# Kernel tuning notes

Measured on AMD Instinct MI355X. Metric: run time of the kernel, lower is better.

Reference implementation:

```python
import jax, jax.numpy as jnp
import numpy as np

D_MODEL = 256
N_HEADS = 4
SPARSITY_RATIO = 0.5
B, N, E = 4, 2048, 65536


def setup_inputs() -> dict:
    key = jax.random.key(0)
    ks = jax.random.split(key, 16)
    d, h = D_MODEL, D_MODEL // 2
    s = 1.0 / np.sqrt(d)
    inp = {
        "x": jax.random.normal(ks[0], (B, N, d), dtype=jnp.float32),
        "edge_index": jax.random.randint(ks[1], (2, E), 0, N, dtype=jnp.int64),
        "Wq": jax.random.uniform(ks[2], (d, d), minval=-s, maxval=s),
        "bq": jnp.zeros((d,), jnp.float32),
        "Wk": jax.random.uniform(ks[3], (d, d), minval=-s, maxval=s),
        "bk": jnp.zeros((d,), jnp.float32),
        "Wv": jax.random.uniform(ks[4], (d, d), minval=-s, maxval=s),
        "bv": jnp.zeros((d,), jnp.float32),
        "Wo": jax.random.uniform(ks[5], (d, d), minval=-s, maxval=s),
        "bo": jnp.zeros((d,), jnp.float32),
        "Wg1": jax.random.uniform(ks[6], (d, h), minval=-s, maxval=s),  # gnn conv1 (in,out)
        "bg1": jnp.zeros((h,), jnp.float32),
        "Wg2": jax.random.uniform(ks[7], (h, 1), minval=-s, maxval=s),  # gnn conv2
        "bg2": jnp.zeros((1,), jnp.float32),
    }
    return inp


def reference(x, edge_index, Wq, bq, Wk, bk, Wv, bv, Wo, bo, Wg1, bg1, Wg2, bg2):
    b, n, d = x.shape
    hd = d // N_HEADS
    row, col = edge_index[0], edge_index[1]

    # Lightweight GNN topo scores, vmapped over batch (replaces python loop)
    def gnn(xb):
        aggr = jax.ops.segment_sum(xb[col], row, num_segments=n)  # [N, d]
        hdn = jax.nn.relu(aggr @ Wg1 + bg1)
        return (hdn @ Wg2 + bg2)[:, 0]  # [N]

    topo_scores = jax.vmap(gnn)(x)  # [B, N]

    Q = (x @ Wq + bq).reshape(b, n, N_HEADS, hd)
    K = (x @ Wk + bk).reshape(b, n, N_HEADS, hd)
    V = (x @ Wv + bv).reshape(b, n, N_HEADS, hd)

    content_scores = jnp.einsum('bnhd,bmhd->bhnm', Q, K) / np.sqrt(hd)
    content_attn = jax.nn.softmax(content_scores, axis=-1)  # [B,H,N,N]

    # Edge mask (identical across batch, assignment semantics => set)
    edge_mask = jnp.zeros((n, n), jnp.float32).at[row, col].set(1.0)

    # top-k columns per batch (same columns for every query row i)
    k = max(1, int(n * (1 - SPARSITY_RATIO)))
    _, topk_idx = jax.lax.top_k(topo_scores, k)  # [B, k]
    col_mask = jnp.zeros((b, n), jnp.float32).at[jnp.arange(b)[:, None], topk_idx].set(1.0)

    sparse_mask = jnp.maximum(edge_mask[None, :, :], col_mask[:, None, :])  # [B,N,N]
    mask4 = jnp.broadcast_to(sparse_mask[:, None, :, :], (b, N_HEADS, n, n))

    sparse_attn = content_attn * mask4
    sparse_attn = sparse_attn / (jnp.sum(sparse_attn, axis=-1, keepdims=True) + 1e-8)

    out = jnp.einsum('bhnm,bmhd->bnhd', sparse_attn, V).reshape(b, n, d)
    out = out @ Wo + bo
    return out, mask4
```

## Files before the change

### kernel.cpp

```cpp
#include <hip/hip_runtime.h>
#include <hip/hip_bf16.h>
#include <stdint.h>

#define NTOK 2048
#define NB 4
#define DM 256
#define HD 64
#define NE 65536
#define SCAP 128
#define NKSL 4
#define LIVE_ROWS 6272

typedef __bf16 bf16x8 __attribute__((ext_vector_type(8)));
typedef float f32x4 __attribute__((ext_vector_type(4)));

#define MFMA16 __builtin_amdgcn_mfma_f32_16x16x32_bf16

__device__ __forceinline__ unsigned short f2bf(float f) {
    union { float f; uint32_t u; } v; v.f = f;
    return (unsigned short)((v.u + 0x7fffu + ((v.u >> 16) & 1u)) >> 16);
}

__global__ __launch_bounds__(256) void k_prep(const float* __restrict__ x,
                       unsigned short* __restrict__ xb,
                       const float* __restrict__ W0, const float* __restrict__ W1,
                       const float* __restrict__ W2, const float* __restrict__ W3,
                       unsigned short* __restrict__ WT, float4* __restrict__ wsz,
                       const float* __restrict__ Wg1, float* __restrict__ y) {
    __shared__ float xs[16][256];
    int bid = blockIdx.x, t = threadIdx.x;
    if (bid < 132) {
        wsz[bid * 256 + t] = float4{0.f, 0.f, 0.f, 0.f};
    } else if (bid < 1156) {
        int b2 = bid - 132;
        int sel = b2 >> 8;
        const float* W = sel == 0 ? W0 : sel == 1 ? W1 : sel == 2 ? W2 : W3;
        int e = (b2 & 255) * 256 + t;
        int n = e >> 8, k = e & 255;
        WT[sel * 65536 + e] = f2bf(W[k * 256 + n]);
    } else {
        int m0 = (bid - 1156) * 16;
        #pragma unroll
        for (int j = 0; j < 16; ++j) {
            float v = x[(size_t)(m0 + j) * DM + t];
            xs[j][t] = v;
            xb[(size_t)(m0 + j) * DM + t] = f2bf(v);
        }
        __syncthreads();
        int c = t & 127, g = t >> 7;
        float acc[8] = {0.f, 0.f, 0.f, 0.f, 0.f, 0.f, 0.f, 0.f};
        const float* xr = &xs[g * 8][0];
        #pragma unroll 4
        for (int r = 0; r < DM; ++r) {
            float w = Wg1[r * 128 + c];
            #pragma unroll
            for (int j = 0; j < 8; ++j) acc[j] += xr[j * 256 + r] * w;
        }
        #pragma unroll
        for (int j = 0; j < 8; ++j) y[(size_t)(m0 + g * 8 + j) * 128 + c] = acc[j];
    }
}

__global__ void k_edges(const int* __restrict__ ei, uint32_t* __restrict__ cursor,
                        uint32_t* __restrict__ scol, uint32_t* __restrict__ ebits) {
    int e = blockIdx.x * 256 + threadIdx.x;
    int r = ei[e];
    int c = ei[NE + e];
    uint32_t slot = atomicAdd(&cursor[r], 1u);
    if (slot < SCAP) scol[r * SCAP + slot] = (uint32_t)c;
    atomicOr(&ebits[r * 64 + (c >> 5)], 1u << (c & 31));
}

__global__ __launch_bounds__(256) void k_gnn_qkv(
    const float* __restrict__ y, const uint32_t* __restrict__ cursor,
    const uint32_t* __restrict__ scol,
    const float* __restrict__ bg1, const float* __restrict__ Wg2,
    const float* __restrict__ bg2, float* __restrict__ topo,
    const unsigned short* __restrict__ xbf, const unsigned short* __restrict__ WT,
    const float* __restrict__ bq, const float* __restrict__ bk, const float* __restrict__ bv,
    unsigned short* __restrict__ qo, unsigned short* __restrict__ kt,
    unsigned short* __restrict__ vt3) {
    int bid = blockIdx.x, t = threadIdx.x;
    if (bid < 2048) {
        int i = bid;
        int d = t & 127, bp = t >> 7;
        uint32_t cnt = cursor[i]; if (cnt > SCAP) cnt = SCAP;
        const uint32_t* sc = scol + i * SCAP;
        const float* yA = y + (size_t)(bp * NTOK) * 128 + d;
        const float* yB = y + (size_t)((bp + 2) * NTOK) * 128 + d;
        double A0 = 0, A1 = 0, A2 = 0, A3 = 0;
        double B0 = 0, B1 = 0, B2 = 0, B3 = 0;
        uint32_t e = 0;
        for (; e + 3 < cnt; e += 4) {
            int c0 = sc[e] << 7, c1 = sc[e + 1] << 7;
            int c2 = sc[e + 2] << 7, c3 = sc[e + 3] << 7;
            A0 += (double)yA[c0]; A1 += (double)yA[c1];
            A2 += (double)yA[c2]; A3 += (double)yA[c3];
            B0 += (double)yB[c0]; B1 += (double)yB[c1];
            B2 += (double)yB[c2]; B3 += (double)yB[c3];
        }
        for (; e < cnt; ++e) {
            int c0 = sc[e] << 7;
            A0 += (double)yA[c0];
            B0 += (double)yB[c0];
        }
        double hA = (A0 + A1) + (A2 + A3) + (double)bg1[d];
        double hB = (B0 + B1) + (B2 + B3) + (double)bg1[d];
        double w2 = (double)Wg2[d];
        double vA = (hA > 0 ? hA : 0.0) * w2;
        double vB = (hB > 0 ? hB : 0.0) * w2;
        #pragma unroll
        for (int s = 32; s >= 1; s >>= 1) {
            vA += __shfl_xor(vA, s);
            vB += __shfl_xor(vB, s);
        }
        __shared__ double red[4][2];
        int wid = t >> 6;
        if ((t & 63) == 0) { red[wid][0] = vA; red[wid][1] = vB; }
        __syncthreads();
        if (t == 0) {
            double bb = (double)bg2[0];
            topo[0 * NTOK + i] = (float)(red[0][0] + red[1][0] + bb);
            topo[2 * NTOK + i] = (float)(red[0][1] + red[1][1] + bb);
            topo[1 * NTOK + i] = (float)(red[2][0] + red[3][0] + bb);
            topo[3 * NTOK + i] = (float)(red[2][1] + red[3][1] + bb);
        }
    } else {
        int b2 = bid - 2048;
        int z = b2 >> 9, r2 = b2 & 511;
        const unsigned short* W = WT + z * 65536;
        const float* bias = z == 0 ? bq : z == 1 ? bk : bv;

        int lane = t & 63, w = t >> 6;
        int l15 = lane & 15, grp = lane >> 4;
        int mbase = (r2 & 127) * 64 + w * 16;
        int nbase = (r2 >> 7) * 64;
        f32x4 acc0 = {0,0,0,0}, acc1 = {0,0,0,0}, acc2 = {0,0,0,0}, acc3 = {0,0,0,0};
        const unsigned short* ap = xbf + (size_t)(mbase + l15) * DM + grp * 8;
        const unsigned short* bp2 = W + (size_t)(nbase + l15) * DM + grp * 8;
        #pragma unroll
        for (int k0 = 0; k0 < DM; k0 += 32) {
            bf16x8 af = *(const bf16x8*)(ap + k0);
            acc0 = MFMA16(af, *(const bf16x8*)(bp2 + k0), acc0, 0, 0, 0);
            acc1 = MFMA16(af, *(const bf16x8*)(bp2 + 16 * DM + k0), acc1, 0, 0, 0);
            acc2 = MFMA16(af, *(const bf16x8*)(bp2 + 32 * DM + k0), acc2, 0, 0, 0);
            acc3 = MFMA16(af, *(const bf16x8*)(bp2 + 48 * DM + k0), acc3, 0, 0, 0);
        }
        f32x4 accs[4] = {acc0, acc1, acc2, acc3};
        #pragma unroll
        for (int ct = 0; ct < 4; ++ct) {
            #pragma unroll
            for (int r = 0; r < 4; ++r) {
                int m = mbase + grp * 4 + r;
                int n = nbase + ct * 16 + l15;
                float v = accs[ct][r] + bias[n];
                if (z == 0) {
                    qo[(size_t)m * DM + n] = f2bf(v);
                } else {
                    int b = m >> 11, tok = m & 2047, h = n >> 6, d = n & 63;
                    int bh = (b << 2) + h;
                    if (z == 1) {
                        kt[(size_t)bh * 131072 + (tok >> 4) * 1024 + (tok & 15) * 64 + d] = f2bf(v);
                    } else {
                        vt3[(size_t)bh * 131072 + (tok >> 5) * 2048 + d * 32 + (tok & 31)] = f2bf(v);
                    }
                }
            }
        }
    }
}

__global__ __launch_bounds__(256) void k_topk(const float* __restrict__ topo,
                                              uint32_t* __restrict__ colbits) {
    int b = blockIdx.y, t = threadIdx.x;
    int i = blockIdx.x * 256 + t;
    __shared__ float4 sc4[NTOK / 4];
    const float4* tp = (const float4*)(topo + b * NTOK);
    for (int j = t; j < NTOK / 4; j += 256) sc4[j] = tp[j];
    __syncthreads();
    float si = ((const float*)sc4)[i];
    int rank = 0;
    #pragma unroll 2
    for (int jj = 0; jj < NTOK / 4; ++jj) {
        float4 v = sc4[jj];
        int j0 = jj * 4;
        rank += (v.x > si) || (v.x == si && (j0    ) < i);
        rank += (v.y > si) || (v.y == si && (j0 + 1) < i);
        rank += (v.z > si) || (v.z == si && (j0 + 2) < i);
        rank += (v.w > si) || (v.w == si && (j0 + 3) < i);
    }
    unsigned long long m = __ballot(rank < 1024);
    int lane = t & 63;
    if (lane == 0)       colbits[b * 64 + (i >> 5)] = (uint32_t)m;
    else if (lane == 32) colbits[b * 64 + (i >> 5)] = (uint32_t)(m >> 32);
}

__device__ __forceinline__ void mask_row(int rowidx, const uint32_t* __restrict__ eb,
                                         const uint32_t* __restrict__ cb,
                                         float* __restrict__ mout) {
    int t = threadIdx.x;
    int b = rowidx >> 13;
    int i = rowidx & 2047;
    int j0 = t << 3;
    uint32_t mw = eb[i * 64 + (j0 >> 5)] | cb[b * 64 + (j0 >> 5)];
    int sh = j0 & 31;
    float4 v0, v1;
    v0.x = ((mw >> sh) & 1u) ? 1.f : 0.f;
    v0.y = ((mw >> (sh + 1)) & 1u) ? 1.f : 0.f;
    v0.z = ((mw >> (sh + 2)) & 1u) ? 1.f : 0.f;
    v0.w = ((mw >> (sh + 3)) & 1u) ? 1.f : 0.f;
    v1.x = ((mw >> (sh + 4)) & 1u) ? 1.f : 0.f;
    v1.y = ((mw >> (sh + 5)) & 1u) ? 1.f : 0.f;
    v1.z = ((mw >> (sh + 6)) & 1u) ? 1.f : 0.f;
    v1.w = ((mw >> (sh + 7)) & 1u) ? 1.f : 0.f;
    float* p = mout + (size_t)rowidx * NTOK + j0;
    *(float4*)p = v0;
    *(float4*)(p + 4) = v1;
}

__global__ __launch_bounds__(256) void k_attn_mask(const unsigned short* __restrict__ Q,
                                                   const unsigned short* __restrict__ KT,
                                                   const unsigned short* __restrict__ VT3,
                                                   const uint32_t* __restrict__ ebits,
                                                   const uint32_t* __restrict__ colbits,
                                                   float* __restrict__ po,
                                                   float* __restrict__ pl,
                                                   float* __restrict__ mout) {
    int bid = blockIdx.x;
    if (bid >= 2048) {
        mask_row(bid - 2048 + LIVE_ROWS, ebits, colbits, mout);
        return;
    }
    int lane = threadIdx.x & 63, w = threadIdx.x >> 6;
    int l15 = lane & 15, grp = lane >> 4;
    int ks = bid >> 9;
    int bh = (bid >> 5) & 15, b = bh >> 2, h = bh & 3;
    int q = (bid & 31) * 64 + w * 16 + l15;

    const unsigned short* qp = Q + (size_t)(b * NTOK + q) * DM + h * HD + grp * 8;
    bf16x8 qf0 = *(const bf16x8*)(qp);
    bf16x8 qf1 = *(const bf16x8*)(qp + 32);
    const unsigned short* kbase = KT + (size_t)bh * 131072 + l15 * 64 + grp * 8;
    const unsigned short* vbase = VT3 + (size_t)bh * 131072 + l15 * 32 + grp * 8;
    const uint32_t* eb = ebits + q * 64;
    const uint32_t* cbp = colbits + b * 64;

    f32x4 o0 = {0,0,0,0}, o1 = {0,0,0,0}, o2 = {0,0,0,0}, o3 = {0,0,0,0};
    float psum = 0.f;

    int kb0 = ks * (NTOK / NKSL);
    for (int kb = kb0; kb < kb0 + NTOK / NKSL; kb += 32) {
        const unsigned short* kp0 = kbase + (kb >> 4) * 1024;
        f32x4 st0 = {0,0,0,0}, st1 = {0,0,0,0};
        st0 = MFMA16(*(const bf16x8*)(kp0), qf0, st0, 0, 0, 0);
        st0 = MFMA16(*(const bf16x8*)(kp0 + 32), qf1, st0, 0, 0, 0);
        st1 = MFMA16(*(const bf16x8*)(kp0 + 1024), qf0, st1, 0, 0, 0);
        st1 = MFMA16(*(const bf16x8*)(kp0 + 1024 + 32), qf1, st1, 0, 0, 0);

        uint32_t mw = eb[kb >> 5] | cbp[kb >> 5];
        float p[8];
        #pragma unroll
        for (int r = 0; r < 4; ++r) {
            int p0 = grp * 4 + r;
            p[r]     = ((mw >> p0) & 1u)        ? __expf(st0[r] * 0.125f - 8.0f) : 0.f;
            p[4 + r] = ((mw >> (16 + p0)) & 1u) ? __expf(st1[r] * 0.125f - 8.0f) : 0.f;
        }
        #pragma unroll
        for (int j = 0; j < 8; ++j) psum += p[j];

        uint32_t pk00, pk01, pk10, pk11;
        asm("v_cvt_pk_bf16_f32 %0, %1, %2" : "=v"(pk00) : "v"(p[0]), "v"(p[1]));
        asm("v_cvt_pk_bf16_f32 %0, %1, %2" : "=v"(pk01) : "v"(p[2]), "v"(p[3]));
        asm("v_cvt_pk_bf16_f32 %0, %1, %2" : "=v"(pk10) : "v"(p[4]), "v"(p[5]));
        asm("v_cvt_pk_bf16_f32 %0, %1, %2" : "=v"(pk11) : "v"(p[6]), "v"(p[7]));
        union { uint32_t u[4]; bf16x8 v; } pf;
        #pragma unroll
        for (int wi = 0; wi < 4; ++wi) {
            int src = (((grp * 2 + (wi >> 1)) & 3) << 4) | l15;
            uint32_t lo = (uint32_t)__shfl((int)((wi & 1) ? pk01 : pk00), src);
            uint32_t hi = (uint32_t)__shfl((int)((wi & 1) ? pk11 : pk10), src);
            pf.u[wi] = (lane >= 32) ? hi : lo;
        }

        const unsigned short* vk = vbase + (kb >> 5) * 2048;
        o0 = MFMA16(*(const bf16x8*)(vk),            pf.v, o0, 0, 0, 0);
        o1 = MFMA16(*(const bf16x8*)(vk + 16 * 32),  pf.v, o1, 0, 0, 0);
        o2 = MFMA16(*(const bf16x8*)(vk + 32 * 32),  pf.v, o2, 0, 0, 0);
        o3 = MFMA16(*(const bf16x8*)(vk + 48 * 32),  pf.v, o3, 0, 0, 0);
    }
    psum += __shfl_xor(psum, 16);
    psum += __shfl_xor(psum, 32);

    float* pb = po + (((size_t)(ks * 16 + bh) * NTOK + q) * HD);
    *(f32x4*)(pb + 0 * 16 + grp * 4) = o0;
    *(f32x4*)(pb + 1 * 16 + grp * 4) = o1;
    *(f32x4*)(pb + 2 * 16 + grp * 4) = o2;
    *(f32x4*)(pb + 3 * 16 + grp * 4) = o3;
    if (grp == 0) pl[(size_t)(ks * 16 + bh) * NTOK + q] = psum;
}

__global__ __launch_bounds__(256) void k_fin(const float* __restrict__ po,
                                             const float* __restrict__ pl,
                                             unsigned short* __restrict__ aoutb) {
    const size_t SL = (size_t)16 * NTOK * HD;
    const size_t SLP = (size_t)16 * NTOK;
    int tid = blockIdx.x * 256 + threadIdx.x;
    int dc = tid & 7;
    int q = (tid >> 3) & 2047;
    int bh = tid >> 14;
    size_t rb = ((size_t)bh * NTOK + q) * HD + dc * 8;
    float4 s0 = *(const float4*)(po + rb);
    float4 s1 = *(const float4*)(po + rb + 4);
    #pragma unroll
    for (int ks = 1; ks < NKSL; ++ks) {
        float4 a = *(const float4*)(po + ks * SL + rb);
        float4 c = *(const float4*)(po + ks * SL + rb + 4);
        s0.x += a.x; s0.y += a.y; s0.z += a.z; s0.w += a.w;
        s1.x += c.x; s1.y += c.y; s1.z += c.z; s1.w += c.w;
    }
    float l = 0.f;
    #pragma unroll
    for (int ks = 0; ks < NKSL; ++ks) l += pl[ks * SLP + (size_t)bh * NTOK + q];
    float inv = 1.f / l;
    int b = bh >> 2, h = bh & 3;
    union { ushort4 u4[2]; uint4 v; } out;
    out.u4[0].x = f2bf(s0.x * inv); out.u4[0].y = f2bf(s0.y * inv);
    out.u4[0].z = f2bf(s0.z * inv); out.u4[0].w = f2bf(s0.w * inv);
    out.u4[1].x = f2bf(s1.x * inv); out.u4[1].y = f2bf(s1.y * inv);
    out.u4[1].z = f2bf(s1.z * inv); out.u4[1].w = f2bf(s1.w * inv);
    *(uint4*)(aoutb + ((size_t)(b * NTOK + q) * DM) + h * HD + dc * 8) = out.v;
}

__global__ __launch_bounds__(256) void k_gemm_o(const unsigned short* __restrict__ A,
                                                const unsigned short* __restrict__ WT,
                                                const float* __restrict__ bias,
                                                float* __restrict__ out) {
    int bid = blockIdx.x;
    int lane = threadIdx.x & 63, w = threadIdx.x >> 6;
    int l15 = lane & 15, grp = lane >> 4;
    int mbase = (bid & 127) * 64 + w * 16;
    int nbase = (bid >> 7) * 64;
    f32x4 acc0 = {0,0,0,0}, acc1 = {0,0,0,0}, acc2 = {0,0,0,0}, acc3 = {0,0,0,0};
    const unsigned short* ap = A + (size_t)(mbase + l15) * DM + grp * 8;
    const unsigned short* bp = WT + (size_t)(nbase + l15) * DM + grp * 8;
    #pragma unroll
    for (int k0 = 0; k0 < DM; k0 += 32) {
        bf16x8 af = *(const bf16x8*)(ap + k0);
        acc0 = MFMA16(af, *(const bf16x8*)(bp + k0), acc0, 0, 0, 0);
        acc1 = MFMA16(af, *(const bf16x8*)(bp + 16 * DM + k0), acc1, 0, 0, 0);
        acc2 = MFMA16(af, *(const bf16x8*)(bp + 32 * DM + k0), acc2, 0, 0, 0);
        acc3 = MFMA16(af, *(const bf16x8*)(bp + 48 * DM + k0), acc3, 0, 0, 0);
    }
    f32x4 accs[4] = {acc0, acc1, acc2, acc3};
    #pragma unroll
    for (int ct = 0; ct < 4; ++ct) {
        #pragma unroll
        for (int r = 0; r < 4; ++r) {
            int m = mbase + grp * 4 + r;
            int n = nbase + ct * 16 + l15;
            out[(size_t)m * DM + n] = accs[ct][r] + bias[n];
        }
    }
}

__global__ void k_mask4b(const uint32_t* __restrict__ ebits, const uint32_t* __restrict__ colbits,
                         float* __restrict__ mout) {
    mask_row(blockIdx.x, ebits, colbits, mout);
}

extern "C" void kernel_launch(void* const* d_in, const int* in_sizes, int n_in,
                              void* d_out, int out_size, void* d_ws, size_t ws_size,
                              hipStream_t stream) {
    const float* x   = (const float*)d_in[0];
    const int*   ei  = (const int*)d_in[1];
    const float* Wq  = (const float*)d_in[2];
    const float* bq  = (const float*)d_in[3];
    const float* Wk  = (const float*)d_in[4];
    const float* bk  = (const float*)d_in[5];
    const float* Wv  = (const float*)d_in[6];
    const float* bv  = (const float*)d_in[7];
    const float* Wo  = (const float*)d_in[8];
    const float* bo  = (const float*)d_in[9];
    const float* Wg1 = (const float*)d_in[10];
    const float* bg1 = (const float*)d_in[11];
    const float* Wg2 = (const float*)d_in[12];
    const float* bg2 = (const float*)d_in[13];

    float* out0  = (float*)d_out;
    float* mask4 = out0 + (size_t)NB * NTOK * DM;

    uint8_t* big = (uint8_t*)mask4;
    unsigned short* qbf   = (unsigned short*)(big);
    unsigned short* kt    = (unsigned short*)(big + (4u  << 20));
    unsigned short* vt3   = (unsigned short*)(big + (8u  << 20));
    unsigned short* wt    = (unsigned short*)(big + (12u << 20));
    unsigned short* aoutb = (unsigned short*)(big + (12u << 20) + (512u << 10));
    float*          po    = (float*)(big + (16u << 20) + (512u << 10));
    float*          pl    = (float*)(big + (48u << 20) + (512u << 10));
    unsigned short* xbf   = (unsigned short*)(big + (49u << 20));
    uint32_t*       scol  = (uint32_t*)(big + (53u << 20));
    float*          y     = (float*)(big + (54u << 20));

    uint8_t* ws = (uint8_t*)d_ws;
    uint32_t* cursor  = (uint32_t*)(ws);
    uint32_t* ebits   = (uint32_t*)(ws + (16u << 10));
    uint32_t* colbits = (uint32_t*)(ws + (528u << 10));
    float*    topo    = (float*)(ws + (532u << 10));

    k_prep<<<1668, 256, 0, stream>>>(x, xbf, Wq, Wk, Wv, Wo, wt, (float4*)ws, Wg1, y);
    k_edges<<<256, 256, 0, stream>>>(ei, cursor, scol, ebits);
    k_gnn_qkv<<<3584, 256, 0, stream>>>(y, cursor, scol, bg1, Wg2, bg2, topo,
                                        xbf, wt, bq, bk, bv, qbf, kt, vt3);
    k_topk<<<dim3(8, 4), 256, 0, stream>>>(topo, colbits);
    k_attn_mask<<<2048 + (32768 - LIVE_ROWS), 256, 0, stream>>>(qbf, kt, vt3, ebits, colbits,
                                                                po, pl, mask4);
    k_fin<<<1024, 256, 0, stream>>>(po, pl, aoutb);
    k_gemm_o<<<512, 256, 0, stream>>>(aoutb, wt + 196608, bo, out0);
    k_mask4b<<<LIVE_ROWS, 256, 0, stream>>>(ebits, colbits, mask4);
}
```

Before: 302.5 us.

## Stage K/V tiles in swizzled shared memory and write mask once per head-quad

```diff
diff --git a/kernel.cpp b/kernel.cpp
--- a/kernel.cpp
+++ b/kernel.cpp
@@ -9,7 +9,6 @@
 #define NE 65536
 #define SCAP 128
 #define NKSL 4
-#define LIVE_ROWS 6272
 
 typedef __bf16 bf16x8 __attribute__((ext_vector_type(8)));
 typedef float f32x4 __attribute__((ext_vector_type(4)));
@@ -195,43 +194,18 @@
     else if (lane == 32) colbits[b * 64 + (i >> 5)] = (uint32_t)(m >> 32);
 }
 
-__device__ __forceinline__ void mask_row(int rowidx, const uint32_t* __restrict__ eb,
-                                         const uint32_t* __restrict__ cb,
-                                         float* __restrict__ mout) {
-    int t = threadIdx.x;
-    int b = rowidx >> 13;
-    int i = rowidx & 2047;
-    int j0 = t << 3;
-    uint32_t mw = eb[i * 64 + (j0 >> 5)] | cb[b * 64 + (j0 >> 5)];
-    int sh = j0 & 31;
-    float4 v0, v1;
-    v0.x = ((mw >> sh) & 1u) ? 1.f : 0.f;
-    v0.y = ((mw >> (sh + 1)) & 1u) ? 1.f : 0.f;
-    v0.z = ((mw >> (sh + 2)) & 1u) ? 1.f : 0.f;
-    v0.w = ((mw >> (sh + 3)) & 1u) ? 1.f : 0.f;
-    v1.x = ((mw >> (sh + 4)) & 1u) ? 1.f : 0.f;
-    v1.y = ((mw >> (sh + 5)) & 1u) ? 1.f : 0.f;
-    v1.z = ((mw >> (sh + 6)) & 1u) ? 1.f : 0.f;
-    v1.w = ((mw >> (sh + 7)) & 1u) ? 1.f : 0.f;
-    float* p = mout + (size_t)rowidx * NTOK + j0;
-    *(float4*)p = v0;
-    *(float4*)(p + 4) = v1;
-}
-
-__global__ __launch_bounds__(256) void k_attn_mask(const unsigned short* __restrict__ Q,
+__global__ __launch_bounds__(256) void k_attn_part(const unsigned short* __restrict__ Q,
                                                    const unsigned short* __restrict__ KT,
                                                    const unsigned short* __restrict__ VT3,
                                                    const uint32_t* __restrict__ ebits,
                                                    const uint32_t* __restrict__ colbits,
                                                    float* __restrict__ po,
-                                                   float* __restrict__ pl,
-                                                   float* __restrict__ mout) {
+                                                   float* __restrict__ pl) {
+    __shared__ unsigned short ksh[2][2048];
+    __shared__ unsigned short vsh[2][2048];
     int bid = blockIdx.x;
-    if (bid >= 2048) {
-        mask_row(bid - 2048 + LIVE_ROWS, ebits, colbits, mout);
-        return;
-    }
-    int lane = threadIdx.x & 63, w = threadIdx.x >> 6;
+    int t = threadIdx.x;
+    int lane = t & 63, w = t >> 6;
     int l15 = lane & 15, grp = lane >> 4;
     int ks = bid >> 9;
     int bh = (bid >> 5) & 15, b = bh >> 2, h = bh & 3;
@@ -240,22 +214,46 @@
     const unsigned short* qp = Q + (size_t)(b * NTOK + q) * DM + h * HD + grp * 8;
     bf16x8 qf0 = *(const bf16x8*)(qp);
     bf16x8 qf1 = *(const bf16x8*)(qp + 32);
-    const unsigned short* kbase = KT + (size_t)bh * 131072 + l15 * 64 + grp * 8;
-    const unsigned short* vbase = VT3 + (size_t)bh * 131072 + l15 * 32 + grp * 8;
+    const unsigned short* Kt = KT + (size_t)bh * 131072;
+    const unsigned short* Vt = VT3 + (size_t)bh * 131072;
     const uint32_t* eb = ebits + q * 64;
     const uint32_t* cbp = colbits + b * 64;
 
+    int kb0 = ks * (NTOK / NKSL);
+
+    int kso = (t * 16) ^ (((t >> 3) & 7) << 4);
+    int vso = (t * 16) ^ (((t >> 2) & 7) << 4);
+    int swz = (l15 & 7) << 4;
+
+    {
+        uint4 kv = *(const uint4*)(Kt + (size_t)(kb0 >> 4) * 1024 + t * 8);
+        *(uint4*)((char*)&ksh[0][0] + kso) = kv;
+        uint4 vv = *(const uint4*)(Vt + (size_t)(kb0 >> 5) * 2048 + t * 8);
+        *(uint4*)((char*)&vsh[0][0] + vso) = vv;
+    }
+    __syncthreads();
+
     f32x4 o0 = {0,0,0,0}, o1 = {0,0,0,0}, o2 = {0,0,0,0}, o3 = {0,0,0,0};
     float psum = 0.f;
 
-    int kb0 = ks * (NTOK / NKSL);
-    for (int kb = kb0; kb < kb0 + NTOK / NKSL; kb += 32) {
-        const unsigned short* kp0 = kbase + (kb >> 4) * 1024;
+    for (int it = 0; it < NTOK / NKSL / 32; ++it) {
+        int buf = it & 1;
+        if (it + 1 < NTOK / NKSL / 32) {
+            int kb = kb0 + (it + 1) * 32;
+            uint4 kv = *(const uint4*)(Kt + (size_t)(kb >> 4) * 1024 + t * 8);
+            *(uint4*)((char*)&ksh[buf ^ 1][0] + kso) = kv;
+            uint4 vv = *(const uint4*)(Vt + (size_t)(kb >> 5) * 2048 + t * 8);
+            *(uint4*)((char*)&vsh[buf ^ 1][0] + vso) = vv;
+        }
+        int kb = kb0 + it * 32;
+        const char* kp = (const char*)&ksh[buf][0];
+        const char* vp = (const char*)&vsh[buf][0];
+
         f32x4 st0 = {0,0,0,0}, st1 = {0,0,0,0};
-        st0 = MFMA16(*(const bf16x8*)(kp0), qf0, st0, 0, 0, 0);
-        st0 = MFMA16(*(const bf16x8*)(kp0 + 32), qf1, st0, 0, 0, 0);
-        st1 = MFMA16(*(const bf16x8*)(kp0 + 1024), qf0, st1, 0, 0, 0);
-        st1 = MFMA16(*(const bf16x8*)(kp0 + 1024 + 32), qf1, st1, 0, 0, 0);
+        st0 = MFMA16(*(const bf16x8*)(kp + ((l15 * 128 + grp * 16) ^ swz)),        qf0, st0, 0, 0, 0);
+        st0 = MFMA16(*(const bf16x8*)(kp + ((l15 * 128 + 64 + grp * 16) ^ swz)),   qf1, st0, 0, 0, 0);
+        st1 = MFMA16(*(const bf16x8*)(kp + (((16 + l15) * 128 + grp * 16) ^ swz)), qf0, st1, 0, 0, 0);
+        st1 = MFMA16(*(const bf16x8*)(kp + (((16 + l15) * 128 + 64 + grp * 16) ^ swz)), qf1, st1, 0, 0, 0);
 
         uint32_t mw = eb[kb >> 5] | cbp[kb >> 5];
         float p[8];
@@ -282,11 +280,11 @@
             pf.u[wi] = (lane >= 32) ? hi : lo;
         }
 
-        const unsigned short* vk = vbase + (kb >> 5) * 2048;
-        o0 = MFMA16(*(const bf16x8*)(vk),            pf.v, o0, 0, 0, 0);
-        o1 = MFMA16(*(const bf16x8*)(vk + 16 * 32),  pf.v, o1, 0, 0, 0);
-        o2 = MFMA16(*(const bf16x8*)(vk + 32 * 32),  pf.v, o2, 0, 0, 0);
-        o3 = MFMA16(*(const bf16x8*)(vk + 48 * 32),  pf.v, o3, 0, 0, 0);
+        o0 = MFMA16(*(const bf16x8*)(vp + ((l15 * 64 + grp * 16) ^ swz)),          pf.v, o0, 0, 0, 0);
+        o1 = MFMA16(*(const bf16x8*)(vp + (((16 + l15) * 64 + grp * 16) ^ swz)),   pf.v, o1, 0, 0, 0);
+        o2 = MFMA16(*(const bf16x8*)(vp + (((32 + l15) * 64 + grp * 16) ^ swz)),   pf.v, o2, 0, 0, 0);
+        o3 = MFMA16(*(const bf16x8*)(vp + (((48 + l15) * 64 + grp * 16) ^ swz)),   pf.v, o3, 0, 0, 0);
+        __syncthreads();
     }
     psum += __shfl_xor(psum, 16);
     psum += __shfl_xor(psum, 32);
@@ -329,6 +327,38 @@
     out.u4[1].x = f2bf(s1.x * inv); out.u4[1].y = f2bf(s1.y * inv);
     out.u4[1].z = f2bf(s1.z * inv); out.u4[1].w = f2bf(s1.w * inv);
     *(uint4*)(aoutb + ((size_t)(b * NTOK + q) * DM) + h * HD + dc * 8) = out.v;
+}
+
+__device__ __forceinline__ void mask_quad(int idx, const uint32_t* __restrict__ eb,
+                                          const uint32_t* __restrict__ cb,
+                                          float* __restrict__ mout) {
+    int b = idx >> 19;
+    int rem = idx & 524287;
+    int i = rem >> 8;
+    int j = (rem & 255) << 3;
+    uint32_t mw = eb[i * 64 + (j >> 5)] | cb[b * 64 + (j >> 5)];
+    int sh = j & 31;
+    float4 v0, v1;
+    v0.x = ((mw >> sh) & 1u) ? 1.f : 0.f;
+    v0.y = ((mw >> (sh + 1)) & 1u) ? 1.f : 0.f;
+    v0.z = ((mw >> (sh + 2)) & 1u) ? 1.f : 0.f;
+    v0.w = ((mw >> (sh + 3)) & 1u) ? 1.f : 0.f;
+    v1.x = ((mw >> (sh + 4)) & 1u) ? 1.f : 0.f;
+    v1.y = ((mw >> (sh + 5)) & 1u) ? 1.f : 0.f;
+    v1.z = ((mw >> (sh + 6)) & 1u) ? 1.f : 0.f;
+    v1.w = ((mw >> (sh + 7)) & 1u) ? 1.f : 0.f;
+    size_t base = (((size_t)b * 4) * NTOK + i) * NTOK + j;
+    #pragma unroll
+    for (int hh = 0; hh < 4; ++hh) {
+        float* p = mout + base + (size_t)hh * NTOK * NTOK;
+        *(float4*)p = v0;
+        *(float4*)(p + 4) = v1;
+    }
+}
+
+__global__ void k_mask4(const uint32_t* __restrict__ ebits, const uint32_t* __restrict__ colbits,
+                        float* __restrict__ mout) {
+    mask_quad(blockIdx.x * 256 + threadIdx.x, ebits, colbits, mout);
 }
 
 __global__ __launch_bounds__(256) void k_gemm_o(const unsigned short* __restrict__ A,
@@ -363,11 +393,6 @@
     }
 }
 
-__global__ void k_mask4b(const uint32_t* __restrict__ ebits, const uint32_t* __restrict__ colbits,
-                         float* __restrict__ mout) {
-    mask_row(blockIdx.x, ebits, colbits, mout);
-}
-
 extern "C" void kernel_launch(void* const* d_in, const int* in_sizes, int n_in,
                               void* d_out, int out_size, void* d_ws, size_t ws_size,
                               hipStream_t stream) {
@@ -395,11 +420,11 @@
     unsigned short* vt3   = (unsigned short*)(big + (8u  << 20));
     unsigned short* wt    = (unsigned short*)(big + (12u << 20));
     unsigned short* aoutb = (unsigned short*)(big + (12u << 20) + (512u << 10));
-    float*          po    = (float*)(big + (16u << 20) + (512u << 10));
-    float*          pl    = (float*)(big + (48u << 20) + (512u << 10));
-    unsigned short* xbf   = (unsigned short*)(big + (49u << 20));
-    uint32_t*       scol  = (uint32_t*)(big + (53u << 20));
-    float*          y     = (float*)(big + (54u << 20));
+    uint32_t*       scol  = (uint32_t*)      (big + (16u << 20) + (512u << 10));
+    unsigned short* xbf   = (unsigned short*)(big + (17u << 20) + (512u << 10));
+    float*          y     = (float*)         (big + (21u << 20) + (512u << 10));
+    float*          po    = (float*)         (big + (25u << 20) + (512u << 10));
+    float*          pl    = (float*)         (big + (57u << 20) + (512u << 10));
 
     uint8_t* ws = (uint8_t*)d_ws;
     uint32_t* cursor  = (uint32_t*)(ws);
@@ -412,9 +437,8 @@
     k_gnn_qkv<<<3584, 256, 0, stream>>>(y, cursor, scol, bg1, Wg2, bg2, topo,
                                         xbf, wt, bq, bk, bv, qbf, kt, vt3);
     k_topk<<<dim3(8, 4), 256, 0, stream>>>(topo, colbits);
-    k_attn_mask<<<2048 + (32768 - LIVE_ROWS), 256, 0, stream>>>(qbf, kt, vt3, ebits, colbits,
-                                                                po, pl, mask4);
+    k_attn_part<<<NKSL * 512, 256, 0, stream>>>(qbf, kt, vt3, ebits, colbits, po, pl);
     k_fin<<<1024, 256, 0, stream>>>(po, pl, aoutb);
     k_gemm_o<<<512, 256, 0, stream>>>(aoutb, wt + 196608, bo, out0);
-    k_mask4b<<<LIVE_ROWS, 256, 0, stream>>>(ebits, colbits, mask4);
-}
+    k_mask4<<<8192, 256, 0, stream>>>(ebits, colbits, mask4);
+}
```

After: 251.2 us. 16.9% less time.
